# Kernel tuning notes

Measured on AMD Instinct MI355X. Metric: run time of the kernel, lower is better.

Reference implementation:

```python
import jax, jax.numpy as jnp
import numpy as np

N, E = 50000, 800000
F_IN, C_PRE, C, G_HID = 16, 32, 64, 64
EPS = 1e-5


def graph_norm(x, batch, w, b, ms):
    # PyG GraphNorm over a single graph (batch all zeros)
    cnt = jax.ops.segment_sum(jnp.ones((x.shape[0], 1), x.dtype), batch, num_segments=1)
    mean = jax.ops.segment_sum(x, batch, num_segments=1) / cnt
    out = x - mean[batch] * ms
    var = jax.ops.segment_sum(out * out, batch, num_segments=1) / cnt
    std = jnp.sqrt(var + EPS)
    return w * out / std[batch] + b


def ggnn_conv(h, edge_index, edge_attr,
              gw1, gb1, gw2, gb2, gw3, gb3,
              zw, zb, rw, rb, hw, hb):
    n = h.shape[0]
    loops = jnp.arange(n)
    row = jnp.concatenate([edge_index[0], loops])  # sources (x_j)
    col = jnp.concatenate([edge_index[1], loops])  # targets (x_i), aggregation index
    ea = jnp.concatenate([edge_attr, jnp.ones((n, 1), h.dtype)], axis=0)
    deg = jax.ops.segment_sum(jnp.ones(col.shape[0], h.dtype), col, num_segments=n)
    dis = jnp.where(deg > 0, deg ** -0.5, 0.0)
    norm = dis[row] * dis[col]
    x_j = h[row]
    x_i = h[col]
    g = jnp.concatenate([x_i, x_j, ea], axis=-1)            # [E+N, 2C+1]
    g = jax.nn.relu(g @ gw1 + gb1)
    g = jax.nn.relu(g @ gw2 + gb2)
    gate = jax.nn.sigmoid(g @ gw3 + gb3)                     # [E+N, 1]
    msg = gate * (norm[:, None] * x_j)
    aggr = jax.ops.segment_sum(msg, col, num_segments=n)     # scatter-add
    zi = jnp.concatenate([h, aggr], axis=-1)
    z = jax.nn.sigmoid(zi @ zw + zb)
    r = jax.nn.sigmoid(zi @ rw + rb)
    hc = jax.nn.relu(jnp.concatenate([r * h, aggr], axis=-1) @ hw + hb)
    return (1.0 - z) * h + z * hc


def setup_inputs() -> dict:
    key = jax.random.key(0)
    ks = iter(jax.random.split(key, 40))

    def lin(k, fi, fo):
        return jax.random.normal(k, (fi, fo), jnp.float32) / np.sqrt(fi)

    inp = {
        'x': jax.random.normal(next(ks), (N, F_IN), jnp.float32),
        'edge_index': jax.random.randint(next(ks), (2, E), 0, N),
        'edge_attr': jax.random.uniform(next(ks), (E, 1), jnp.float32),
        'batch': jnp.zeros((N,), jnp.int32),
        'preproc_w': lin(next(ks), F_IN, C_PRE), 'preproc_b': jnp.zeros((C_PRE,), jnp.float32),
        'gn_pre_w': jnp.ones((C_PRE,), jnp.float32), 'gn_pre_b': jnp.zeros((C_PRE,), jnp.float32), 'gn_pre_ms': jnp.ones((C_PRE,), jnp.float32),
        'init_w': lin(next(ks), C_PRE, C), 'init_b': jnp.zeros((C,), jnp.float32),
        'gn_init_w': jnp.ones((C,), jnp.float32), 'gn_init_b': jnp.zeros((C,), jnp.float32), 'gn_init_ms': jnp.ones((C,), jnp.float32),
        'gate_w1': lin(next(ks), 2 * C + 1, G_HID), 'gate_b1': jnp.zeros((G_HID,), jnp.float32),
        'gate_w2': lin(next(ks), G_HID, G_HID), 'gate_b2': jnp.zeros((G_HID,), jnp.float32),
        'gate_w3': lin(next(ks), G_HID, 1), 'gate_b3': jnp.zeros((1,), jnp.float32),
        'lin_z_w': lin(next(ks), 2 * C, C), 'lin_z_b': jnp.zeros((C,), jnp.float32),
        'lin_r_w': lin(next(ks), 2 * C, C), 'lin_r_b': jnp.zeros((C,), jnp.float32),
        'lin_h_w': lin(next(ks), 2 * C, C), 'lin_h_b': jnp.zeros((C,), jnp.float32),
        'gn_ggnn_w': jnp.ones((C,), jnp.float32), 'gn_ggnn_b': jnp.zeros((C,), jnp.float32), 'gn_ggnn_ms': jnp.ones((C,), jnp.float32),
        'fc1_w': lin(next(ks), 2 * C, C), 'fc1_b': jnp.zeros((C,), jnp.float32),
        'gn_fc1_w': jnp.ones((C,), jnp.float32), 'gn_fc1_b': jnp.zeros((C,), jnp.float32), 'gn_fc1_ms': jnp.ones((C,), jnp.float32),
        'fc2_w': lin(next(ks), C, 2), 'fc2_b': jnp.zeros((2,), jnp.float32),
    }
    return inp


def reference(x, edge_index, edge_attr, batch,
              preproc_w, preproc_b, gn_pre_w, gn_pre_b, gn_pre_ms,
              init_w, init_b, gn_init_w, gn_init_b, gn_init_ms,
              gate_w1, gate_b1, gate_w2, gate_b2, gate_w3, gate_b3,
              lin_z_w, lin_z_b, lin_r_w, lin_r_b, lin_h_w, lin_h_b,
              gn_ggnn_w, gn_ggnn_b, gn_ggnn_ms,
              fc1_w, fc1_b, gn_fc1_w, gn_fc1_b, gn_fc1_ms,
              fc2_w, fc2_b):
    n_layers = 4
    h = x @ preproc_w + preproc_b
    h = graph_norm(h, batch, gn_pre_w, gn_pre_b, gn_pre_ms)
    h = jax.nn.relu(h)
    h0 = h @ init_w + init_b
    h0 = graph_norm(h0, batch, gn_init_w, gn_init_b, gn_init_ms)
    h0 = jax.nn.relu(h0)
    h = h0
    for _ in range(n_layers):  # tied GGNN layer
        h = ggnn_conv(h, edge_index, edge_attr,
                      gate_w1, gate_b1, gate_w2, gate_b2, gate_w3, gate_b3,
                      lin_z_w, lin_z_b, lin_r_w, lin_r_b, lin_h_w, lin_h_b)
        h = graph_norm(h, batch, gn_ggnn_w, gn_ggnn_b, gn_ggnn_ms)
    out = jnp.concatenate([h0, h], axis=1)
    out = out @ fc1_w + fc1_b
    out = graph_norm(out, batch, gn_fc1_w, gn_fc1_b, gn_fc1_ms)
    out = jax.nn.relu(out)
    out = out @ fc2_w + fc2_b  # [N, 2] logits
    return out
```

## Files before the change

kernel.cpp:

```cpp
#include <hip/hip_runtime.h>

#define GN_EPS 1e-5f

typedef _Float16 half8 __attribute__((ext_vector_type(8)));
typedef float floatx4 __attribute__((ext_vector_type(4)));

__device__ __forceinline__ float sigmoidf_(float x){ return 1.0f/(1.0f+__expf(-x)); }
__device__ __forceinline__ float bcast_(float v, int k){
  return __int_as_float(__builtin_amdgcn_readlane(__float_as_int(v), k));
}

__global__ void cnt_init_kernel(int* cnt, int n){
  int i = blockIdx.x*blockDim.x+threadIdx.x;
  if (i < n) cnt[i] = 1;
}
__global__ void cnt_kernel(const int* __restrict__ ei, int* cnt, int E){
  int e = blockIdx.x*blockDim.x+threadIdx.x;
  if (e < E) atomicAdd(&cnt[ei[E+e]], 1);
}
__global__ void dis_from_cnt_kernel(const int* __restrict__ cnt, float* dis, int n){
  int i = blockIdx.x*blockDim.x+threadIdx.x;
  if (i < n) dis[i] = rsqrtf((float)cnt[i]);
}
__global__ __launch_bounds__(256) void scan1_kernel(const int* __restrict__ cnt,
                                                    int* loc, int* bsum, int n){
  __shared__ int s[256];
  int t = threadIdx.x, i = blockIdx.x*256 + t;
  int v = (i < n) ? cnt[i] : 0;
  s[t] = v; __syncthreads();
  #pragma unroll
  for (int d = 1; d < 256; d <<= 1){
    int u = (t >= d) ? s[t-d] : 0; __syncthreads();
    s[t] += u; __syncthreads();
  }
  if (i < n) loc[i] = s[t] - v;
  if (t == 255) bsum[blockIdx.x] = s[255];
}
__global__ __launch_bounds__(256) void scan2_kernel(int* bsum, int nb){
  __shared__ int s[256];
  int t = threadIdx.x;
  int v = (t < nb) ? bsum[t] : 0;
  s[t] = v; __syncthreads();
  #pragma unroll
  for (int d = 1; d < 256; d <<= 1){
    int u = (t >= d) ? s[t-d] : 0; __syncthreads();
    s[t] += u; __syncthreads();
  }
  if (t < nb) bsum[t] = s[t] - v;
}
__global__ void scan3_kernel(const int* __restrict__ loc, const int* __restrict__ bsum,
                             int* rowptr, int n, int total){
  int i = blockIdx.x*blockDim.x+threadIdx.x;
  if (i < n) rowptr[i] = loc[i] + bsum[i >> 8];
  if (i == 0) rowptr[n] = total;
}
__global__ void scatter_kernel(const int* __restrict__ ei, const float* __restrict__ ea,
                               const int* __restrict__ rowptr, int* fill,
                               unsigned* sd, _Float16* ea2, int E, int n){
  int idx = blockIdx.x*blockDim.x+threadIdx.x;
  int tot = E + n;
  if (idx >= tot) return;
  int r, c; float v;
  if (idx < E){ r = ei[idx]; c = ei[E+idx]; v = ea[idx]; }
  else        { r = c = idx - E; v = 1.0f; }
  int j = rowptr[c] + atomicAdd(&fill[c], 1);
  sd[j] = (unsigned)r | ((unsigned)c << 16);
  ea2[j] = (_Float16)v;
}

__global__ __launch_bounds__(256) void wprep_kernel(
    const float* __restrict__ w1, const float* __restrict__ zw,
    const float* __restrict__ rw, const float* __restrict__ hw,
    const float* __restrict__ fw, const float* __restrict__ w2,
    _Float16* __restrict__ wp){
  int idx = blockIdx.x*256 + threadIdx.x;
  if (idx < 8192){
    int t=idx>>10, kh=(idx>>9)&1, g=(idx>>7)&3, l=(idx>>3)&15, j=idx&7;
    int kg=(t>=4?64:0)+kh*32+g*8+j;
    wp[idx] = (_Float16)w1[kg*64 + (t&3)*16 + l];
  } else if (idx < 40960){
    int m=(idx-8192)>>13, k=(idx-8192)&8191;
    int t=(k>>11)&3, kh=(k>>9)&3, g=(k>>7)&3, l=(k>>3)&15, j=k&7;
    const float* W = (m==0)?zw:((m==1)?rw:((m==2)?hw:fw));
    wp[idx] = (_Float16)W[(kh*32+g*8+j)*64 + t*16 + l];
  } else if (idx < 45056){
    int k = idx-40960;
    int t=(k>>10)&3, kh=(k>>9)&1, g=(k>>7)&3, l=(k>>3)&15, j=k&7;
    wp[idx] = (_Float16)w2[(kh*32+g*8+j)*64 + t*16 + l];
  }
}

template<int K_IN, int C_OUT>
__global__ __launch_bounds__(256) void mm1_kernel(
    const float* __restrict__ x, const float* __restrict__ W,
    const float* __restrict__ b, float* __restrict__ y, int n){
  __shared__ float sW[K_IN*C_OUT];
  for (int i = threadIdx.x; i < K_IN*C_OUT; i += 256) sW[i] = W[i];
  __syncthreads();
  const int lane = threadIdx.x & 63;
  const int col  = (lane < C_OUT) ? lane : 0;
  const float bias = b[col];
  int wid = (blockIdx.x*256 + threadIdx.x) >> 6;
  int nw  = (gridDim.x*256) >> 6;
  for (int i = wid; i < n; i += nw){
    float xv = (lane < K_IN) ? x[(size_t)i*K_IN + lane] : 0.0f;
    float a0 = bias, a1 = 0.0f;
    #pragma unroll
    for (int k = 0; k < K_IN; k += 2){
      a0 += bcast_(xv, k  ) * sW[(k  )*C_OUT + col];
      a1 += bcast_(xv, k+1) * sW[(k+1)*C_OUT + col];
    }
    if (lane < C_OUT) y[(size_t)i*C_OUT + lane] = a0 + a1;
  }
}

__global__ __launch_bounds__(256) void pq_mfma_kernel(
    const _Float16* __restrict__ QH, const _Float16* __restrict__ w1p,
    const float* __restrict__ b1, _Float16* __restrict__ Ph,
    _Float16* __restrict__ QHq, int n)
{
  __shared__ _Float16 sB[8192];
  for (int i = threadIdx.x; i < 1024; i += 256)
    ((half8*)sB)[i] = ((const half8*)w1p)[i];
  __syncthreads();
  const int lane = threadIdx.x & 63;
  const int g16 = lane>>4, l16 = lane&15;
  float b1f[4];
  #pragma unroll
  for (int t = 0; t < 4; ++t) b1f[t] = b1[t*16 + l16];

  int wid = (blockIdx.x*blockDim.x + threadIdx.x) >> 6;
  int nw  = (gridDim.x*blockDim.x) >> 6;
  int tiles = (n + 15) >> 4;
  for (int tile = wid; tile < tiles; tile += nw){
    int base = tile*16;
    int na = min(base + l16, n-1);
    half8 af0 = *(const half8*)(QH + (size_t)na*128 + 64 + g16*8);
    half8 af1 = *(const half8*)(QH + (size_t)na*128 + 96 + g16*8);
    floatx4 acc[8];
    #pragma unroll
    for (int t = 0; t < 8; ++t){
      float bv = (t < 4) ? b1f[t] : 0.0f;
      acc[t] = (floatx4){bv, bv, bv, bv};
    }
    #pragma unroll
    for (int t = 0; t < 8; ++t){
      half8 bf0 = *(const half8*)&sB[((t*2+0)*4+g16)*128 + l16*8];
      half8 bf1 = *(const half8*)&sB[((t*2+1)*4+g16)*128 + l16*8];
      acc[t] = __builtin_amdgcn_mfma_f32_16x16x32_f16(af0, bf0, acc[t], 0, 0, 0);
      acc[t] = __builtin_amdgcn_mfma_f32_16x16x32_f16(af1, bf1, acc[t], 0, 0, 0);
    }
    #pragma unroll
    for (int t = 0; t < 8; ++t)
      #pragma unroll
      for (int rg = 0; rg < 4; ++rg){
        int nd = base + g16*4 + rg;
        if (nd < n){
          if (t < 4) Ph [(size_t)nd*64  + t*16 + l16]     = (_Float16)acc[t][rg];
          else       QHq[(size_t)nd*128 + (t-4)*16 + l16] = (_Float16)acc[t][rg];
        }
      }
  }
}

__global__ __launch_bounds__(256) void gru_mfma_kernel(
    float* __restrict__ h, const float* __restrict__ aggr,
    const float* __restrict__ dis, const _Float16* __restrict__ QH,
    const _Float16* __restrict__ gwp,
    const float* __restrict__ zb, const float* __restrict__ rb,
    const float* __restrict__ hb,
    float* __restrict__ stats, int n)
{
  __shared__ _Float16 sW[3*8192];
  __shared__ _Float16 sRH[4][16][72];
  __shared__ float sSt[128];
  if (threadIdx.x < 128) sSt[threadIdx.x] = 0.f;
  for (int i = threadIdx.x; i < 3072; i += 256)
    ((half8*)sW)[i] = ((const half8*)gwp)[i];
  __syncthreads();
  const int lane = threadIdx.x & 63;
  const int g16 = lane>>4, l16 = lane&15;
  const int w = threadIdx.x >> 6;
  float zbf[4], rbf[4], hbf[4];
  #pragma unroll
  for (int t = 0; t < 4; ++t){
    zbf[t] = zb[t*16+l16]; rbf[t] = rb[t*16+l16]; hbf[t] = hb[t*16+l16];
  }
  float ssum[4] = {0,0,0,0}, ssq[4] = {0,0,0,0};
#define GW(m,t,kh) (*(const half8*)&sW[(m)*8192 + (((t)*4+(kh))*4+g16)*128 + l16*8])

  int wid = (blockIdx.x*blockDim.x + threadIdx.x) >> 6;
  int nw  = (gridDim.x*blockDim.x) >> 6;
  int tiles = (n + 15) >> 4;
  for (int tile = wid; tile < tiles; tile += nw){
    int base = tile*16;
    int na = min(base + l16, n-1);
    float dv = dis[na];
    half8 af[4];
    af[0] = *(const half8*)(QH + (size_t)na*128 + 64 + g16*8);
    af[1] = *(const half8*)(QH + (size_t)na*128 + 96 + g16*8);
    #pragma unroll
    for (int kh = 0; kh < 2; ++kh){
      const float* ar = aggr + (size_t)na*64 + kh*32 + g16*8;
      float4 a0 = *(const float4*)ar;
      float4 a1 = *(const float4*)(ar+4);
      half8 t8;
      t8[0]=(_Float16)(a0.x*dv); t8[1]=(_Float16)(a0.y*dv);
      t8[2]=(_Float16)(a0.z*dv); t8[3]=(_Float16)(a0.w*dv);
      t8[4]=(_Float16)(a1.x*dv); t8[5]=(_Float16)(a1.y*dv);
      t8[6]=(_Float16)(a1.z*dv); t8[7]=(_Float16)(a1.w*dv);
      af[2+kh] = t8;
    }
    floatx4 az[4], ar4[4];
    #pragma unroll
    for (int t = 0; t < 4; ++t){
      az[t]  = (floatx4){zbf[t], zbf[t], zbf[t], zbf[t]};
      ar4[t] = (floatx4){rbf[t], rbf[t], rbf[t], rbf[t]};
      #pragma unroll
      for (int kh = 0; kh < 4; ++kh){
        az[t]  = __builtin_amdgcn_mfma_f32_16x16x32_f16(af[kh], GW(0,t,kh), az[t],  0, 0, 0);
        ar4[t] = __builtin_amdgcn_mfma_f32_16x16x32_f16(af[kh], GW(1,t,kh), ar4[t], 0, 0, 0);
      }
    }
    float zr[16], hv[16];
    #pragma unroll
    for (int t = 0; t < 4; ++t)
      #pragma unroll
      for (int rg = 0; rg < 4; ++rg){
        int ndc = min(base + g16*4 + rg, n-1);
        float hval = h[(size_t)ndc*64 + t*16 + l16];
        float zv = sigmoidf_(az[t][rg]);
        float rv = sigmoidf_(ar4[t][rg]);
        zr[t*4+rg] = zv; hv[t*4+rg] = hval;
        sRH[w][g16*4+rg][t*16+l16] = (_Float16)(rv*hval);
      }
    asm volatile("s_waitcnt lgkmcnt(0)" ::: "memory");
    __builtin_amdgcn_sched_barrier(0);
    half8 af2_0 = *(const half8*)&sRH[w][l16][g16*8];
    half8 af2_1 = *(const half8*)&sRH[w][l16][32 + g16*8];
    floatx4 ah[4];
    #pragma unroll
    for (int t = 0; t < 4; ++t){
      ah[t] = (floatx4){hbf[t], hbf[t], hbf[t], hbf[t]};
      ah[t] = __builtin_amdgcn_mfma_f32_16x16x32_f16(af2_0, GW(2,t,0), ah[t], 0, 0, 0);
      ah[t] = __builtin_amdgcn_mfma_f32_16x16x32_f16(af2_1, GW(2,t,1), ah[t], 0, 0, 0);
      ah[t] = __builtin_amdgcn_mfma_f32_16x16x32_f16(af[2],  GW(2,t,2), ah[t], 0, 0, 0);
      ah[t] = __builtin_amdgcn_mfma_f32_16x16x32_f16(af[3],  GW(2,t,3), ah[t], 0, 0, 0);
    }
    #pragma unroll
    for (int t = 0; t < 4; ++t)
      #pragma unroll
      for (int rg = 0; rg < 4; ++rg){
        int nd = base + g16*4 + rg;
        if (nd < n){
          float hc = fmaxf(ah[t][rg], 0.f);
          float zv = zr[t*4+rg];
          float hn = (1.f - zv)*hv[t*4+rg] + zv*hc;
          h[(size_t)nd*64 + t*16 + l16] = hn;
          ssum[t] += hn; ssq[t] += hn*hn;
        }
      }
  }
#undef GW
  #pragma unroll
  for (int t = 0; t < 4; ++t){
    atomicAdd(&sSt[t*16+l16], ssum[t]);
    atomicAdd(&sSt[64+t*16+l16], ssq[t]);
  }
  __syncthreads();
  if (threadIdx.x < 128) atomicAdd(&stats[threadIdx.x], sSt[threadIdx.x]);
}

__global__ __launch_bounds__(256) void fc1_mfma_kernel(
    const float* __restrict__ h0, const float* __restrict__ h,
    const _Float16* __restrict__ fp, const float* __restrict__ b,
    float* __restrict__ out, float* __restrict__ stats, int n)
{
  __shared__ _Float16 sB[8192];
  __shared__ float sSt[128];
  if (threadIdx.x < 128) sSt[threadIdx.x] = 0.f;
  for (int i = threadIdx.x; i < 1024; i += 256)
    ((half8*)sB)[i] = ((const half8*)fp)[i];
  __syncthreads();
  const int lane = threadIdx.x & 63;
  const int g16 = lane>>4, l16 = lane&15;
  float bf[4];
  #pragma unroll
  for (int t = 0; t < 4; ++t) bf[t] = b[t*16+l16];
  float ssum[4] = {0,0,0,0}, ssq[4] = {0,0,0,0};

  int wid = (blockIdx.x*blockDim.x + threadIdx.x) >> 6;
  int nw  = (gridDim.x*blockDim.x) >> 6;
  int tiles = (n + 15) >> 4;
  for (int tile = wid; tile < tiles; tile += nw){
    int base = tile*16;
    int na = min(base + l16, n-1);
    half8 af[4];
    #pragma unroll
    for (int kh = 0; kh < 4; ++kh){
      const float* sp = (kh < 2 ? h0 : h) + (size_t)na*64 + (kh&1)*32 + g16*8;
      float4 a0 = *(const float4*)sp;
      float4 a1 = *(const float4*)(sp+4);
      half8 t8;
      t8[0]=(_Float16)a0.x; t8[1]=(_Float16)a0.y; t8[2]=(_Float16)a0.z; t8[3]=(_Float16)a0.w;
      t8[4]=(_Float16)a1.x; t8[5]=(_Float16)a1.y; t8[6]=(_Float16)a1.z; t8[7]=(_Float16)a1.w;
      af[kh] = t8;
    }
    #pragma unroll
    for (int t = 0; t < 4; ++t){
      floatx4 acc = (floatx4){bf[t], bf[t], bf[t], bf[t]};
      #pragma unroll
      for (int kh = 0; kh < 4; ++kh)
        acc = __builtin_amdgcn_mfma_f32_16x16x32_f16(af[kh],
                *(const half8*)&sB[((t*4+kh)*4+g16)*128 + l16*8], acc, 0, 0, 0);
      #pragma unroll
      for (int rg = 0; rg < 4; ++rg){
        int nd = base + g16*4 + rg;
        if (nd < n){
          float v = acc[rg];
          out[(size_t)nd*64 + t*16 + l16] = v;
          ssum[t] += v; ssq[t] += v*v;
        }
      }
    }
  }
  #pragma unroll
  for (int t = 0; t < 4; ++t){
    atomicAdd(&sSt[t*16+l16], ssum[t]);
    atomicAdd(&sSt[64+t*16+l16], ssq[t]);
  }
  __syncthreads();
  if (threadIdx.x < 128) atomicAdd(&stats[threadIdx.x], sSt[threadIdx.x]);
}

__global__ __launch_bounds__(256) void edge_tile_kernel(
    const unsigned* __restrict__ sd, const _Float16* __restrict__ ea2,
    const _Float16* __restrict__ Ph, const _Float16* __restrict__ QH,
    const float* __restrict__ dis,
    const _Float16* __restrict__ w2p, const float* __restrict__ b2,
    const float* __restrict__ w1e, const float* __restrict__ w3,
    const float* __restrict__ b3,
    float* __restrict__ aggr, int EN)
{
  const int lane = threadIdx.x & 63;
  const int g16  = lane >> 4;
  const int l16  = lane & 15;

  half8 bfrag[4][2];
  #pragma unroll
  for (int t = 0; t < 4; ++t)
    #pragma unroll
    for (int kh = 0; kh < 2; ++kh)
      bfrag[t][kh] = *(const half8*)&w2p[t*1024 + kh*512 + g16*128 + l16*8];

  float w1f[16];
  #pragma unroll
  for (int kh = 0; kh < 2; ++kh)
    #pragma unroll
    for (int j = 0; j < 8; ++j)
      w1f[kh*8+j] = w1e[kh*32 + g16*8 + j];

  float w3f[4], b2f[4];
  #pragma unroll
  for (int t = 0; t < 4; ++t){ w3f[t] = w3[t*16 + l16]; b2f[t] = b2[t*16 + l16]; }
  const float b3v = b3[0];
  const _Float16* QHh = QH + 64;

  int wid = (blockIdx.x*blockDim.x + threadIdx.x) >> 6;
  int nw  = (gridDim.x*blockDim.x) >> 6;
  int tiles = (EN + 15) >> 4;

  for (int tile = wid; tile < tiles; tile += nw){
    int e0 = tile << 4;
    int m = EN - e0; if (m > 16) m = 16;
    int el = e0 + ((l16 < m) ? l16 : (m-1));
    unsigned sdv = sd[el];
    int r = (int)(sdv & 0xffffu);
    int c = (int)(sdv >> 16);
    float eav = (float)ea2[el];
    float dv  = dis[r];

    half8 hq0 = *(const half8*)(QH + (size_t)r*128 + g16*8);
    half8 hq1 = *(const half8*)(QH + (size_t)r*128 + 32 + g16*8);
    half8 p0  = *(const half8*)(Ph + (size_t)c*64 + g16*8);
    half8 p1  = *(const half8*)(Ph + (size_t)c*64 + 32 + g16*8);

    _Float16 hv16[16];
    #pragma unroll
    for (int i = 0; i < 16; ++i){
      int ri = __builtin_amdgcn_readlane(r, i);
      hv16[i] = QHh[(size_t)ri*128 + lane];
    }

    half8 afrag[2];
    #pragma unroll
    for (int j8 = 0; j8 < 8; ++j8){
      afrag[0][j8] = (_Float16)fmaxf((float)p0[j8] + (float)hq0[j8] + eav*w1f[j8],   0.0f);
      afrag[1][j8] = (_Float16)fmaxf((float)p1[j8] + (float)hq1[j8] + eav*w1f[8+j8], 0.0f);
    }

    floatx4 acc[4];
    #pragma unroll
    for (int t4 = 0; t4 < 4; ++t4)
      acc[t4] = (floatx4){b2f[t4], b2f[t4], b2f[t4], b2f[t4]};
    __builtin_amdgcn_s_setprio(1);
    #pragma unroll
    for (int t4 = 0; t4 < 4; ++t4){
      acc[t4] = __builtin_amdgcn_mfma_f32_16x16x32_f16(afrag[0], bfrag[t4][0], acc[t4], 0, 0, 0);
      acc[t4] = __builtin_amdgcn_mfma_f32_16x16x32_f16(afrag[1], bfrag[t4][1], acc[t4], 0, 0, 0);
    }
    __builtin_amdgcn_s_setprio(0);

    float s[4] = {0.f,0.f,0.f,0.f};
    #pragma unroll
    for (int t4 = 0; t4 < 4; ++t4)
      #pragma unroll
      for (int rg = 0; rg < 4; ++rg)
        s[rg] += fmaxf(acc[t4][rg], 0.0f) * w3f[t4];
    #pragma unroll
    for (int rg = 0; rg < 4; ++rg){
      #pragma unroll
      for (int off = 1; off < 16; off <<= 1)
        s[rg] += __shfl_xor(s[rg], off);
      s[rg] = sigmoidf_(s[rg] + b3v);
    }

    float accv = 0.f;
    #pragma unroll
    for (int i = 0; i < 16; ++i){
      float gi = bcast_(s[i & 3], (i >> 2) * 16);
      float fv = (i < m) ? gi * bcast_(dv, i) : 0.0f;
      accv += fv * (float)hv16[i];
      int ci = __builtin_amdgcn_readlane(c, i);
      int cn = (i < 15) ? __builtin_amdgcn_readlane(c, i+1) : -1;
      if (cn != ci){
        atomicAdd(&aggr[(size_t)ci*64 + lane], accv);
        accv = 0.f;
      }
    }
  }
}

template<int C>
__global__ __launch_bounds__(256) void norm_stats_kernel(
    const float* __restrict__ x, int n, float* __restrict__ stats){
  __shared__ float ssum[256], ssq[256];
  const int tid = threadIdx.x;
  const int c = tid % C;
  int row = (blockIdx.x*256 + tid) / C;
  int stride = (gridDim.x*256) / C;
  float s = 0.f, q = 0.f;
  for (int i = row; i < n; i += stride){
    float v = x[(size_t)i*C + c];
    s += v; q += v*v;
  }
  ssum[tid] = s; ssq[tid] = q;
  __syncthreads();
  if (tid < C){
    float S = 0.f, Q2 = 0.f;
    for (int t = tid; t < 256; t += C){ S += ssum[t]; Q2 += ssq[t]; }
    atomicAdd(&stats[tid], S);
    atomicAdd(&stats[C + tid], Q2);
  }
}

template<int C, int RELU, int DUAL, int H16>
__global__ __launch_bounds__(256) void norm_apply_kernel(
    const float* __restrict__ x, const float* __restrict__ stats,
    const float* __restrict__ w, const float* __restrict__ b,
    const float* __restrict__ ms, float* __restrict__ y,
    float* __restrict__ y2, _Float16* __restrict__ hh, int n){
  const float invN = 1.0f / (float)n;
  size_t idx = blockIdx.x*256 + threadIdx.x;
  size_t step = (size_t)gridDim.x*256;
  size_t tot = (size_t)n*C;
  for (; idx < tot; idx += step){
    int c = idx % C;
    float mean = stats[c] * invN;
    float mm = mean * ms[c];
    float var = stats[C + c]*invN - mm*(2.0f*mean - mm);
    float inv = rsqrtf(fmaxf(var, 0.0f) + GN_EPS);
    float v = (x[idx] - mm)*inv*w[c] + b[c];
    if (RELU) v = fmaxf(v, 0.0f);
    y[idx] = v;
    if (DUAL) y2[idx] = v;
    if (H16) hh[(idx >> 6)*128 + 64 + (idx & 63)] = (_Float16)v;
  }
}

__global__ void fc2_kernel(
    const float* __restrict__ x, const float* __restrict__ w,
    const float* __restrict__ b, float* __restrict__ out, int n){
  int i = blockIdx.x*blockDim.x + threadIdx.x;
  if (i >= n) return;
  float a0 = b[0], a1 = b[1];
  const float4* xr = (const float4*)(x + (size_t)i*64);
  #pragma unroll
  for (int k4 = 0; k4 < 16; ++k4){
    float4 v = xr[k4];
    int k = k4*4;
    a0 += v.x*w[(k+0)*2+0] + v.y*w[(k+1)*2+0] + v.z*w[(k+2)*2+0] + v.w*w[(k+3)*2+0];
    a1 += v.x*w[(k+0)*2+1] + v.y*w[(k+1)*2+1] + v.z*w[(k+2)*2+1] + v.w*w[(k+3)*2+1];
  }
  out[i*2+0] = a0;
  out[i*2+1] = a1;
}

extern "C" void kernel_launch(void* const* d_in, const int* in_sizes, int n_in,
                              void* d_out, int out_size, void* d_ws, size_t ws_size,
                              hipStream_t stream){
  const float* x          = (const float*)d_in[0];
  const int*   ei         = (const int*)  d_in[1];
  const float* ea         = (const float*)d_in[2];
  const float* preproc_w  = (const float*)d_in[4];
  const float* preproc_b  = (const float*)d_in[5];
  const float* gn_pre_w   = (const float*)d_in[6];
  const float* gn_pre_b   = (const float*)d_in[7];
  const float* gn_pre_ms  = (const float*)d_in[8];
  const float* init_w     = (const float*)d_in[9];
  const float* init_b     = (const float*)d_in[10];
  const float* gn_init_w  = (const float*)d_in[11];
  const float* gn_init_b  = (const float*)d_in[12];
  const float* gn_init_ms = (const float*)d_in[13];
  const float* gate_w1    = (const float*)d_in[14];
  const float* gate_b1    = (const float*)d_in[15];
  const float* gate_w2    = (const float*)d_in[16];
  const float* gate_b2    = (const float*)d_in[17];
  const float* gate_w3    = (const float*)d_in[18];
  const float* gate_b3    = (const float*)d_in[19];
  const float* lin_z_w    = (const float*)d_in[20];
  const float* lin_z_b    = (const float*)d_in[21];
  const float* lin_r_w    = (const float*)d_in[22];
  const float* lin_r_b    = (const float*)d_in[23];
  const float* lin_h_w    = (const float*)d_in[24];
  const float* lin_h_b    = (const float*)d_in[25];
  const float* gn_ggnn_w  = (const float*)d_in[26];
  const float* gn_ggnn_b  = (const float*)d_in[27];
  const float* gn_ggnn_ms = (const float*)d_in[28];
  const float* fc1_w      = (const float*)d_in[29];
  const float* fc1_b      = (const float*)d_in[30];
  const float* gn_fc1_w   = (const float*)d_in[31];
  const float* gn_fc1_b   = (const float*)d_in[32];
  const float* gn_fc1_ms  = (const float*)d_in[33];
  const float* fc2_w      = (const float*)d_in[34];
  const float* fc2_b      = (const float*)d_in[35];

  const int N = in_sizes[3];
  const int E = in_sizes[1] / 2;
  const int EN = E + N;

  float* base = (float*)d_ws;
  const size_t R = (size_t)64*N;
  float* h     = base;
  float* h0    = h    + R;
  float* Preg  = h0   + R;
  float* aggr  = Preg + R;
  float* QHreg = aggr + R;
  float* dis   = QHreg + R;
  float* stats = dis + N;
  size_t need = (5*R + N + 128) * sizeof(float);
  if (ws_size < need || N > 65535) return;

  _Float16* Ph  = (_Float16*)Preg;
  _Float16* QH  = (_Float16*)QHreg;
  unsigned* sd  = (unsigned*)(Preg + 32*(size_t)N);
  _Float16* ea2 = (_Float16*)(sd + EN);
  _Float16* wp  = (_Float16*)(((uintptr_t)(ea2 + EN) + 15) & ~(uintptr_t)15);
  _Float16* w1p = wp;
  _Float16* gwp = wp + 8192;
  _Float16* fc1p= wp + 32768;
  _Float16* w2p = wp + 40960;

  int* cnt    = (int*)aggr;
  int* loc    = cnt + N;
  int* fill   = loc + N;
  int* bsum   = fill + N;
  int* rowptr = bsum + 256;

  const int GB = 1024;
  const int RB = 784;
  const int EB = 3072;
  const int nb = (N + 255) / 256;

  cnt_init_kernel<<<(N+255)/256, 256, 0, stream>>>(cnt, N);
  cnt_kernel<<<(E+255)/256, 256, 0, stream>>>(ei, cnt, E);
  dis_from_cnt_kernel<<<(N+255)/256, 256, 0, stream>>>(cnt, dis, N);
  scan1_kernel<<<nb, 256, 0, stream>>>(cnt, loc, bsum, N);
  scan2_kernel<<<1, 256, 0, stream>>>(bsum, nb);
  scan3_kernel<<<nb, 256, 0, stream>>>(loc, bsum, rowptr, N, EN);
  hipMemsetAsync(fill, 0, (size_t)N*sizeof(int), stream);
  scatter_kernel<<<(EN+255)/256, 256, 0, stream>>>(ei, ea, rowptr, fill, sd, ea2, E, N);
  wprep_kernel<<<176, 256, 0, stream>>>(gate_w1, lin_z_w, lin_r_w, lin_h_w, fc1_w, gate_w2, wp);

  mm1_kernel<16,32><<<GB, 256, 0, stream>>>(x, preproc_w, preproc_b, h0, N);
  hipMemsetAsync(stats, 0, 2*64*sizeof(float), stream);
  norm_stats_kernel<32><<<256, 256, 0, stream>>>(h0, N, stats);
  norm_apply_kernel<32,1,0,0><<<2048, 256, 0, stream>>>(h0, stats, gn_pre_w, gn_pre_b, gn_pre_ms, h, nullptr, nullptr, N);

  mm1_kernel<32,64><<<GB, 256, 0, stream>>>(h, init_w, init_b, h0, N);
  hipMemsetAsync(stats, 0, 2*64*sizeof(float), stream);
  norm_stats_kernel<64><<<256, 256, 0, stream>>>(h0, N, stats);
  norm_apply_kernel<64,1,1,1><<<2048, 256, 0, stream>>>(h0, stats, gn_init_w, gn_init_b, gn_init_ms, h0, h, QH, N);

  for (int layer = 0; layer < 4; ++layer){
    pq_mfma_kernel<<<RB, 256, 0, stream>>>(QH, w1p, gate_b1, Ph, QH, N);
    hipMemsetAsync(aggr, 0, R*sizeof(float), stream);
    edge_tile_kernel<<<EB, 256, 0, stream>>>(sd, ea2, Ph, QH, dis,
                                             w2p, gate_b2, gate_w1 + 128*64,
                                             gate_w3, gate_b3, aggr, EN);
    hipMemsetAsync(stats, 0, 2*64*sizeof(float), stream);
    gru_mfma_kernel<<<RB, 256, 0, stream>>>(h, aggr, dis, QH, gwp,
                                            lin_z_b, lin_r_b, lin_h_b, stats, N);
    norm_apply_kernel<64,0,0,1><<<2048, 256, 0, stream>>>(h, stats, gn_ggnn_w, gn_ggnn_b, gn_ggnn_ms, h, nullptr, QH, N);
  }

  hipMemsetAsync(stats, 0, 2*64*sizeof(float), stream);
  fc1_mfma_kernel<<<RB, 256, 0, stream>>>(h0, h, fc1p, fc1_b, aggr, stats, N);
  norm_apply_kernel<64,1,0,0><<<2048, 256, 0, stream>>>(aggr, stats, gn_fc1_w, gn_fc1_b, gn_fc1_ms, h, nullptr, nullptr, N);

  fc2_kernel<<<(N+255)/256, 256, 0, stream>>>(h, fc2_w, fc2_b, (float*)d_out, N);
}
```

Measured before the change: 723.8 us.

## Fuse GraphNorm apply into gate projection and fold buffer zeroing into kernels

The GraphNorm apply step is merged with the per-node gate-projection MFMA kernel (normpq), so normalized h is written and immediately projected without a separate pass over QH. The per-layer memsets go away: gru zeroes aggr after reading it, and the edge kernel clears stats. The edge kernel also computes the first gate layer in packed fp16 arithmetic, precomputes the gate-times-degree scale, and finds segment boundaries with a ballot. This cuts kernel launches and memory passes, at the cost of fp16 precision in the gate's hidden pre-activation and a stats-zeroing race that depends on stream ordering.

After: 631.5 us. 1.15x faster.

```diff
diff --git a/kernel.cpp b/kernel.cpp
--- a/kernel.cpp
+++ b/kernel.cpp
@@ -114,17 +114,40 @@
   }
 }
 
-__global__ __launch_bounds__(256) void pq_mfma_kernel(
-    const _Float16* __restrict__ QH, const _Float16* __restrict__ w1p,
-    const float* __restrict__ b1, _Float16* __restrict__ Ph,
-    _Float16* __restrict__ QHq, int n)
+template<int RELU, int WRITE_H0>
+__global__ __launch_bounds__(256) void normpq_kernel(
+    const float* __restrict__ hin, float* __restrict__ hout,
+    float* __restrict__ h0out,
+    const float* __restrict__ stats,
+    const float* __restrict__ gw, const float* __restrict__ gb,
+    const float* __restrict__ gms,
+    const _Float16* __restrict__ w1p, const float* __restrict__ b1,
+    _Float16* __restrict__ Ph, _Float16* __restrict__ QH, int n)
 {
   __shared__ _Float16 sB[8192];
+  __shared__ float sSO[128];
   for (int i = threadIdx.x; i < 1024; i += 256)
     ((half8*)sB)[i] = ((const half8*)w1p)[i];
+  if (threadIdx.x < 64){
+    int ch = threadIdx.x;
+    float invN = 1.0f/(float)n;
+    float mean = stats[ch]*invN;
+    float mm = mean*gms[ch];
+    float var = stats[64+ch]*invN - mm*(2.0f*mean - mm);
+    float inv = rsqrtf(fmaxf(var,0.f)+GN_EPS);
+    float sc = inv*gw[ch];
+    sSO[ch] = sc;
+    sSO[64+ch] = gb[ch] - mm*sc;
+  }
   __syncthreads();
   const int lane = threadIdx.x & 63;
   const int g16 = lane>>4, l16 = lane&15;
+  float scA[8], ofA[8], scB[8], ofB[8];
+  #pragma unroll
+  for (int j = 0; j < 8; ++j){
+    scA[j]=sSO[g16*8+j];    ofA[j]=sSO[64+g16*8+j];
+    scB[j]=sSO[32+g16*8+j]; ofB[j]=sSO[96+g16*8+j];
+  }
   float b1f[4];
   #pragma unroll
   for (int t = 0; t < 4; ++t) b1f[t] = b1[t*16 + l16];
@@ -135,8 +158,38 @@
   for (int tile = wid; tile < tiles; tile += nw){
     int base = tile*16;
     int na = min(base + l16, n-1);
-    half8 af0 = *(const half8*)(QH + (size_t)na*128 + 64 + g16*8);
-    half8 af1 = *(const half8*)(QH + (size_t)na*128 + 96 + g16*8);
+    const float* hp = hin + (size_t)na*64;
+    float4 a0 = *(const float4*)(hp + g16*8);
+    float4 a1 = *(const float4*)(hp + g16*8 + 4);
+    float4 c0 = *(const float4*)(hp + 32 + g16*8);
+    float4 c1 = *(const float4*)(hp + 32 + g16*8 + 4);
+    float va[8] = {a0.x,a0.y,a0.z,a0.w,a1.x,a1.y,a1.z,a1.w};
+    float vb[8] = {c0.x,c0.y,c0.z,c0.w,c1.x,c1.y,c1.z,c1.w};
+    half8 af0, af1;
+    #pragma unroll
+    for (int j = 0; j < 8; ++j){
+      float v = va[j]*scA[j] + ofA[j];
+      if (RELU) v = fmaxf(v, 0.f);
+      va[j] = v; af0[j] = (_Float16)v;
+      float u = vb[j]*scB[j] + ofB[j];
+      if (RELU) u = fmaxf(u, 0.f);
+      vb[j] = u; af1[j] = (_Float16)u;
+    }
+    float* op = hout + (size_t)na*64;
+    *(float4*)(op + g16*8)       = (float4){va[0],va[1],va[2],va[3]};
+    *(float4*)(op + g16*8 + 4)   = (float4){va[4],va[5],va[6],va[7]};
+    *(float4*)(op + 32 + g16*8)  = (float4){vb[0],vb[1],vb[2],vb[3]};
+    *(float4*)(op + 32 + g16*8+4)= (float4){vb[4],vb[5],vb[6],vb[7]};
+    if (WRITE_H0){
+      float* o2 = h0out + (size_t)na*64;
+      *(float4*)(o2 + g16*8)       = (float4){va[0],va[1],va[2],va[3]};
+      *(float4*)(o2 + g16*8 + 4)   = (float4){va[4],va[5],va[6],va[7]};
+      *(float4*)(o2 + 32 + g16*8)  = (float4){vb[0],vb[1],vb[2],vb[3]};
+      *(float4*)(o2 + 32 + g16*8+4)= (float4){vb[4],vb[5],vb[6],vb[7]};
+    }
+    *(half8*)(QH + (size_t)na*128 + 64 + g16*8) = af0;
+    *(half8*)(QH + (size_t)na*128 + 96 + g16*8) = af1;
+
     floatx4 acc[8];
     #pragma unroll
     for (int t = 0; t < 8; ++t){
@@ -156,15 +209,15 @@
       for (int rg = 0; rg < 4; ++rg){
         int nd = base + g16*4 + rg;
         if (nd < n){
-          if (t < 4) Ph [(size_t)nd*64  + t*16 + l16]     = (_Float16)acc[t][rg];
-          else       QHq[(size_t)nd*128 + (t-4)*16 + l16] = (_Float16)acc[t][rg];
+          if (t < 4) Ph[(size_t)nd*64  + t*16 + l16]      = (_Float16)acc[t][rg];
+          else       QH[(size_t)nd*128 + (t-4)*16 + l16]  = (_Float16)acc[t][rg];
         }
       }
   }
 }
 
 __global__ __launch_bounds__(256) void gru_mfma_kernel(
-    float* __restrict__ h, const float* __restrict__ aggr,
+    float* __restrict__ h, float* __restrict__ aggr,
     const float* __restrict__ dis, const _Float16* __restrict__ QH,
     const _Float16* __restrict__ gwp,
     const float* __restrict__ zb, const float* __restrict__ rb,
@@ -201,9 +254,11 @@
     af[1] = *(const half8*)(QH + (size_t)na*128 + 96 + g16*8);
     #pragma unroll
     for (int kh = 0; kh < 2; ++kh){
-      const float* ar = aggr + (size_t)na*64 + kh*32 + g16*8;
+      float* ar = aggr + (size_t)na*64 + kh*32 + g16*8;
       float4 a0 = *(const float4*)ar;
       float4 a1 = *(const float4*)(ar+4);
+      *(float4*)(ar)   = (float4){0,0,0,0};
+      *(float4*)(ar+4) = (float4){0,0,0,0};
       half8 t8;
       t8[0]=(_Float16)(a0.x*dv); t8[1]=(_Float16)(a0.y*dv);
       t8[2]=(_Float16)(a0.z*dv); t8[3]=(_Float16)(a0.w*dv);
@@ -340,8 +395,10 @@
     const _Float16* __restrict__ w2p, const float* __restrict__ b2,
     const float* __restrict__ w1e, const float* __restrict__ w3,
     const float* __restrict__ b3,
-    float* __restrict__ aggr, int EN)
+    float* __restrict__ aggr, float* __restrict__ stats, int EN)
 {
+  if (blockIdx.x == 0 && threadIdx.x < 128) stats[threadIdx.x] = 0.f;
+
   const int lane = threadIdx.x & 63;
   const int g16  = lane >> 4;
   const int l16  = lane & 15;
@@ -353,12 +410,12 @@
     for (int kh = 0; kh < 2; ++kh)
       bfrag[t][kh] = *(const half8*)&w2p[t*1024 + kh*512 + g16*128 + l16*8];
 
-  float w1f[16];
+  half8 w1h[2];
   #pragma unroll
   for (int kh = 0; kh < 2; ++kh)
     #pragma unroll
     for (int j = 0; j < 8; ++j)
-      w1f[kh*8+j] = w1e[kh*32 + g16*8 + j];
+      w1h[kh][j] = (_Float16)w1e[kh*32 + g16*8 + j];
 
   float w3f[4], b2f[4];
   #pragma unroll
@@ -377,8 +434,8 @@
     unsigned sdv = sd[el];
     int r = (int)(sdv & 0xffffu);
     int c = (int)(sdv >> 16);
-    float eav = (float)ea2[el];
-    float dv  = dis[r];
+    float dv = (l16 < m) ? dis[r] : 0.0f;
+    _Float16 eavh = ea2[el];
 
     half8 hq0 = *(const half8*)(QH + (size_t)r*128 + g16*8);
     half8 hq1 = *(const half8*)(QH + (size_t)r*128 + 32 + g16*8);
@@ -392,11 +449,15 @@
       hv16[i] = QHh[(size_t)ri*128 + lane];
     }
 
-    half8 afrag[2];
-    #pragma unroll
-    for (int j8 = 0; j8 < 8; ++j8){
-      afrag[0][j8] = (_Float16)fmaxf((float)p0[j8] + (float)hq0[j8] + eav*w1f[j8],   0.0f);
-      afrag[1][j8] = (_Float16)fmaxf((float)p1[j8] + (float)hq1[j8] + eav*w1f[8+j8], 0.0f);
+    half8 e8;
+    #pragma unroll
+    for (int j = 0; j < 8; ++j) e8[j] = eavh;
+    half8 a0h = p0 + hq0 + w1h[0]*e8;
+    half8 a1h = p1 + hq1 + w1h[1]*e8;
+    #pragma unroll
+    for (int j = 0; j < 8; ++j){
+      a0h[j] = a0h[j] > (_Float16)0.f ? a0h[j] : (_Float16)0.f;
+      a1h[j] = a1h[j] > (_Float16)0.f ? a1h[j] : (_Float16)0.f;
     }
 
     floatx4 acc[4];
@@ -406,8 +467,8 @@
     __builtin_amdgcn_s_setprio(1);
     #pragma unroll
     for (int t4 = 0; t4 < 4; ++t4){
-      acc[t4] = __builtin_amdgcn_mfma_f32_16x16x32_f16(afrag[0], bfrag[t4][0], acc[t4], 0, 0, 0);
-      acc[t4] = __builtin_amdgcn_mfma_f32_16x16x32_f16(afrag[1], bfrag[t4][1], acc[t4], 0, 0, 0);
+      acc[t4] = __builtin_amdgcn_mfma_f32_16x16x32_f16(a0h, bfrag[t4][0], acc[t4], 0, 0, 0);
+      acc[t4] = __builtin_amdgcn_mfma_f32_16x16x32_f16(a1h, bfrag[t4][1], acc[t4], 0, 0, 0);
     }
     __builtin_amdgcn_s_setprio(0);
 
@@ -425,15 +486,24 @@
       s[rg] = sigmoidf_(s[rg] + b3v);
     }
 
+    float fs[4];
+    #pragma unroll
+    for (int rg = 0; rg < 4; ++rg){
+      float dvp = __shfl(dv, (g16 << 4) | (g16*4 + rg));
+      fs[rg] = s[rg] * dvp;
+    }
+
+    int cnext = __shfl(c, (lane & 48) | ((l16 + 1) & 15));
+    unsigned long long bm = __ballot(c != cnext);
+    unsigned bmask = ((unsigned)bm | 0x8000u) & 0xffffu;
+
     float accv = 0.f;
     #pragma unroll
     for (int i = 0; i < 16; ++i){
-      float gi = bcast_(s[i & 3], (i >> 2) * 16);
-      float fv = (i < m) ? gi * bcast_(dv, i) : 0.0f;
-      accv += fv * (float)hv16[i];
-      int ci = __builtin_amdgcn_readlane(c, i);
-      int cn = (i < 15) ? __builtin_amdgcn_readlane(c, i+1) : -1;
-      if (cn != ci){
+      float gi = bcast_(fs[i & 3], (i >> 2) << 4);
+      accv = fmaf(gi, (float)hv16[i], accv);
+      if ((bmask >> i) & 1){
+        int ci = __builtin_amdgcn_readlane(c, i);
         atomicAdd(&aggr[(size_t)ci*64 + lane], accv);
         accv = 0.f;
       }
@@ -464,12 +534,11 @@
   }
 }
 
-template<int C, int RELU, int DUAL, int H16>
+template<int C, int RELU>
 __global__ __launch_bounds__(256) void norm_apply_kernel(
     const float* __restrict__ x, const float* __restrict__ stats,
     const float* __restrict__ w, const float* __restrict__ b,
-    const float* __restrict__ ms, float* __restrict__ y,
-    float* __restrict__ y2, _Float16* __restrict__ hh, int n){
+    const float* __restrict__ ms, float* __restrict__ y, int n){
   const float invN = 1.0f / (float)n;
   size_t idx = blockIdx.x*256 + threadIdx.x;
   size_t step = (size_t)gridDim.x*256;
@@ -483,8 +552,6 @@
     float v = (x[idx] - mm)*inv*w[c] + b[c];
     if (RELU) v = fmaxf(v, 0.0f);
     y[idx] = v;
-    if (DUAL) y2[idx] = v;
-    if (H16) hh[(idx >> 6)*128 + 64 + (idx & 63)] = (_Float16)v;
   }
 }
 
@@ -591,32 +658,37 @@
   hipMemsetAsync(fill, 0, (size_t)N*sizeof(int), stream);
   scatter_kernel<<<(EN+255)/256, 256, 0, stream>>>(ei, ea, rowptr, fill, sd, ea2, E, N);
   wprep_kernel<<<176, 256, 0, stream>>>(gate_w1, lin_z_w, lin_r_w, lin_h_w, fc1_w, gate_w2, wp);
+  hipMemsetAsync(aggr, 0, R*sizeof(float), stream);
 
   mm1_kernel<16,32><<<GB, 256, 0, stream>>>(x, preproc_w, preproc_b, h0, N);
   hipMemsetAsync(stats, 0, 2*64*sizeof(float), stream);
   norm_stats_kernel<32><<<256, 256, 0, stream>>>(h0, N, stats);
-  norm_apply_kernel<32,1,0,0><<<2048, 256, 0, stream>>>(h0, stats, gn_pre_w, gn_pre_b, gn_pre_ms, h, nullptr, nullptr, N);
+  norm_apply_kernel<32,1><<<2048, 256, 0, stream>>>(h0, stats, gn_pre_w, gn_pre_b, gn_pre_ms, h, N);
 
   mm1_kernel<32,64><<<GB, 256, 0, stream>>>(h, init_w, init_b, h0, N);
   hipMemsetAsync(stats, 0, 2*64*sizeof(float), stream);
   norm_stats_kernel<64><<<256, 256, 0, stream>>>(h0, N, stats);
-  norm_apply_kernel<64,1,1,1><<<2048, 256, 0, stream>>>(h0, stats, gn_init_w, gn_init_b, gn_init_ms, h0, h, QH, N);
+  normpq_kernel<1,1><<<RB, 256, 0, stream>>>(h0, h, h0, stats,
+                                             gn_init_w, gn_init_b, gn_init_ms,
+                                             w1p, gate_b1, Ph, QH, N);
 
   for (int layer = 0; layer < 4; ++layer){
-    pq_mfma_kernel<<<RB, 256, 0, stream>>>(QH, w1p, gate_b1, Ph, QH, N);
-    hipMemsetAsync(aggr, 0, R*sizeof(float), stream);
     edge_tile_kernel<<<EB, 256, 0, stream>>>(sd, ea2, Ph, QH, dis,
                                              w2p, gate_b2, gate_w1 + 128*64,
-                                             gate_w3, gate_b3, aggr, EN);
-    hipMemsetAsync(stats, 0, 2*64*sizeof(float), stream);
+                                             gate_w3, gate_b3, aggr, stats, EN);
     gru_mfma_kernel<<<RB, 256, 0, stream>>>(h, aggr, dis, QH, gwp,
                                             lin_z_b, lin_r_b, lin_h_b, stats, N);
-    norm_apply_kernel<64,0,0,1><<<2048, 256, 0, stream>>>(h, stats, gn_ggnn_w, gn_ggnn_b, gn_ggnn_ms, h, nullptr, QH, N);
+    if (layer < 3)
+      normpq_kernel<0,0><<<RB, 256, 0, stream>>>(h, h, nullptr, stats,
+                                                 gn_ggnn_w, gn_ggnn_b, gn_ggnn_ms,
+                                                 w1p, gate_b1, Ph, QH, N);
+    else
+      norm_apply_kernel<64,0><<<2048, 256, 0, stream>>>(h, stats, gn_ggnn_w, gn_ggnn_b, gn_ggnn_ms, h, N);
   }
 
   hipMemsetAsync(stats, 0, 2*64*sizeof(float), stream);
   fc1_mfma_kernel<<<RB, 256, 0, stream>>>(h0, h, fc1p, fc1_b, aggr, stats, N);
-  norm_apply_kernel<64,1,0,0><<<2048, 256, 0, stream>>>(aggr, stats, gn_fc1_w, gn_fc1_b, gn_fc1_ms, h, nullptr, nullptr, N);
+  norm_apply_kernel<64,1><<<2048, 256, 0, stream>>>(aggr, stats, gn_fc1_w, gn_fc1_b, gn_fc1_ms, h, N);
 
   fc2_kernel<<<(N+255)/256, 256, 0, stream>>>(h, fc2_w, fc2_b, (float*)d_out, N);
 }
```
